# Kernel optimization log

Measured on AMD Instinct MI355X. Metric: run time of the kernel, lower is better.

The kernel has to match this reference:

```python
import jax, jax.numpy as jnp
import numpy as np
import math

H, G, DQK, DV = 16, 4, 64, 128  # n_head, n_kv_group, qk head dim, v head dim


def _rope(t):
    # t: [B, n, T, d] -- standard rotate-half RoPE, base 10000
    B, n, T, d = t.shape
    inv = 1.0 / (10000.0 ** (jnp.arange(0, d, 2, dtype=jnp.float32) / d))  # [d/2]
    ang = jnp.arange(T, dtype=jnp.float32)[:, None] * inv[None, :]          # [T, d/2]
    cos = jnp.concatenate([jnp.cos(ang), jnp.cos(ang)], axis=-1)            # [T, d]
    sin = jnp.concatenate([jnp.sin(ang), jnp.sin(ang)], axis=-1)
    t1, t2 = jnp.split(t, 2, axis=-1)
    rot = jnp.concatenate([-t2, t1], axis=-1)
    return t * cos + rot * sin


def setup_inputs() -> dict:
    key = jax.random.key(0)
    ks = jax.random.split(key, 6)
    B, T, C = 2, 2048, 1024
    x = jax.random.normal(ks[0], (B, T, C), jnp.float32)
    Wq = jax.random.normal(ks[1], (C, H * DQK), jnp.float32) * 0.02
    Wk = jax.random.normal(ks[2], (C, G * DQK), jnp.float32) * 0.02
    Wv = jax.random.normal(ks[3], (C, G * DV), jnp.float32) * 0.02
    Wproj = jax.random.normal(ks[4], (DV, C), jnp.float32) * 0.02
    lobo = jnp.full((H,), 1.0, jnp.float32)  # flash_lobo_log_const per head
    g0 = math.log2(T * T - T)                # qk_norm_factor init from block_size
    qk_norm_factor = jnp.array([g0], dtype=jnp.float32)
    return {"x": x, "iter_num": 0, "Wq": Wq, "Wk": Wk, "Wv": Wv,
            "Wproj": Wproj, "lobo": lobo, "qk_norm_factor": qk_norm_factor}


def reference(x, iter_num, Wq, Wk, Wv, Wproj, lobo, qk_norm_factor):
    B, T, C = x.shape
    # projections (bias=False)
    q = (x @ Wq).reshape(B, T, H, DQK).transpose(0, 2, 1, 3)   # [B,H,T,dqk]
    k = (x @ Wk).reshape(B, T, G, DQK).transpose(0, 2, 1, 3)   # [B,G,T,dqk]
    v = (x @ Wv).reshape(B, T, G, DV).transpose(0, 2, 1, 3)    # [B,G,T,dv]
    # rotary embeddings on q and k
    q = _rope(q)
    k = _rope(k)
    # qk-norm
    q = q / (jnp.linalg.norm(q, axis=-1, keepdims=True) + 1e-6)
    k = k / (jnp.linalg.norm(k, axis=-1, keepdims=True) + 1e-6)
    # learned logit scale: q *= g*sqrt(d), SDPA divides by sqrt(d) -> net scale g
    q = q * (qk_norm_factor[0] * jnp.sqrt(jnp.float32(DQK)))
    # GQA broadcast (repeat_interleave over kv groups)
    rep = H // G
    k = jnp.repeat(k, rep, axis=1)   # [B,H,T,dqk]
    v = jnp.repeat(v, rep, axis=1)   # [B,H,T,dv]
    logits = jnp.einsum('bhqd,bhkd->bhqk', q, k) / jnp.sqrt(jnp.float32(DQK))
    causal = jnp.tril(jnp.ones((T, T), dtype=bool))
    logits = jnp.where(causal[None, None], logits, -jnp.inf)
    # flash-lobo: zero-valued sink key, always visible, logit = per-head bias
    sink = jnp.broadcast_to(lobo[None, :, None, None], (B, H, T, 1))
    att = jax.nn.softmax(jnp.concatenate([sink, logits], axis=-1), axis=-1)
    y = jnp.einsum('bhqk,bhkd->bhqd', att[..., 1:], v)  # sink value is zero
    y = y.sum(axis=1)                                    # head-SUM merge [B,T,dv]
    return y @ Wproj                                     # [B,T,C]
```

## Files before the change

### kernel.cpp

```cpp
#include <hip/hip_runtime.h>
#include <hip/hip_bf16.h>
#include <math.h>

#define B_ 2
#define T_ 2048
#define C_ 1024
#define H_ 16
#define G_ 4
#define DQK_ 64
#define DV_ 128
#define NQKV 1792
#define KS2 2048

typedef __attribute__((ext_vector_type(8))) short short8;
typedef __attribute__((ext_vector_type(4))) float f32x4;
typedef unsigned short ushort_t;

__device__ inline ushort_t f2bf(float f) {
  union { float f; unsigned int u; } v; v.f = f;
  unsigned int r = (v.u + 0x7FFFu + ((v.u >> 16) & 1u)) >> 16;
  return (ushort_t)r;
}
__device__ inline float bf2f(ushort_t h) {
  union { unsigned int u; float f; } v; v.u = ((unsigned int)h) << 16;
  return v.f;
}

#define GLD_LDS16(g, l)                                              \
  __builtin_amdgcn_global_load_lds(                                  \
      (const __attribute__((address_space(1))) void*)(g),            \
      (__attribute__((address_space(3))) void*)(l), 16, 0, 0)

__global__ __launch_bounds__(256) void cast_x(
    const float* __restrict__ x, ushort_t* __restrict__ xb) {
  int idx = blockIdx.x * 256 + threadIdx.x;
  int m = idx >> 7;
  int c8 = idx & 127;
  const float* src = &x[(size_t)m * 1024 + c8 * 8];
  float4 v0 = *(const float4*)&src[0];
  float4 v1 = *(const float4*)&src[4];
  float f[8] = {v0.x, v0.y, v0.z, v0.w, v1.x, v1.y, v1.z, v1.w};
  short8 hv, lv;
#pragma unroll
  for (int c = 0; c < 8; c++) {
    ushort_t h = f2bf(f[c]);
    hv[c] = (short)h;
    lv[c] = (short)f2bf(f[c] - bf2f(h));
  }
  int key = (m >> 1) & 3;
  int phys = (c8 & ~3) * 8 + ((c8 & 3) ^ key) * 8;
  ushort_t* row = xb + (size_t)m * KS2;
  *(short8*)&row[phys] = hv;
  *(short8*)&row[1024 + phys] = lv;
}

__global__ __launch_bounds__(256) void cast_w(
    const float* __restrict__ Wq, const float* __restrict__ Wk,
    const float* __restrict__ Wv, ushort_t* __restrict__ wt) {
  __shared__ float tile[64][65];
  const int n0 = blockIdx.x * 64;
  const int k0 = blockIdx.y * 64;
  const int tid = threadIdx.x;

  const float* Wp; int ldw, noff;
  if (n0 < 1024)      { Wp = Wq; ldw = 1024; noff = n0; }
  else if (n0 < 1280) { Wp = Wk; ldw = 256;  noff = n0 - 1024; }
  else                { Wp = Wv; ldw = 512;  noff = n0 - 1280; }

#pragma unroll
  for (int it = 0; it < 4; it++) {
    int fi = it * 256 + tid;
    int kk = fi >> 4;
    int nc = (fi & 15) * 4;
    float4 v = *(const float4*)&Wp[(size_t)(k0 + kk) * ldw + noff + nc];
    tile[nc + 0][kk] = v.x; tile[nc + 1][kk] = v.y;
    tile[nc + 2][kk] = v.z; tile[nc + 3][kk] = v.w;
  }
  __syncthreads();
  int nn = tid >> 2, seg = tid & 3;
  int n = n0 + nn;
  int key = (n >> 1) & 3;
  ushort_t* row = wt + (size_t)n * KS2;
#pragma unroll
  for (int j = 0; j < 2; j++) {
    short8 hv;
#pragma unroll
    for (int u = 0; u < 8; u++)
      hv[u] = (short)f2bf(tile[nn][seg * 16 + j * 8 + u]);
    int c8 = (k0 >> 3) + seg * 2 + j;
    int phys = (c8 & ~3) * 8 + ((c8 & 3) ^ key) * 8;
    *(short8*)&row[phys] = hv;
  }
}

__global__ __launch_bounds__(256) void cast_wp(
    const float* __restrict__ Wp, ushort_t* __restrict__ wpf) {
  int idx = blockIdx.x * 256 + threadIdx.x;
  int n = idx & 1023;
  int kc = idx >> 10;
  short8 v;
#pragma unroll
  for (int j = 0; j < 8; j++)
    v[j] = (short)f2bf(Wp[(size_t)(kc * 8 + j) * 1024 + n]);
  size_t off = (((size_t)(n >> 7) * 4 + (kc >> 2)) * 8 + ((n >> 4) & 7)) * 512 +
               ((kc & 3) * 16 + (n & 15)) * 8;
  *(short8*)&wpf[off] = v;
}

__global__ __launch_bounds__(256) void gemm_qkv_mfma(
    const ushort_t* __restrict__ xb, const ushort_t* __restrict__ wt,
    float* __restrict__ qkv) {
  __shared__ ushort_t At[128 * 32];
  __shared__ ushort_t Bt[128 * 32];
  const int tid = threadIdx.x;
  const int wave = tid >> 6, lane = tid & 63;
  const int quad = lane >> 4, l16 = lane & 15;
  const int m0 = blockIdx.y * 128, n0 = blockIdx.x * 128;
  const int wm = (wave & 1) * 64, wn = (wave >> 1) * 64;
  const int physq = (quad ^ ((l16 >> 1) & 3)) * 8;
  const int ntiles = (n0 >= 1280) ? 32 : 64;

  f32x4 acc[4][4];
#pragma unroll
  for (int i = 0; i < 4; i++)
#pragma unroll
    for (int j = 0; j < 4; j++) acc[i][j] = (f32x4){0.f, 0.f, 0.f, 0.f};

  const int rA = wave * 32 + (lane >> 2);
  const int cA = (lane & 3) * 8;
  const ushort_t* gA = xb + (size_t)(m0 + rA) * KS2 + cA;
  const ushort_t* gB = wt + (size_t)(n0 + rA) * KS2 + cA;
  ushort_t* lA0 = At + (size_t)(wave * 32) * 32;
  ushort_t* lA1 = At + (size_t)(wave * 32 + 16) * 32;
  ushort_t* lB0 = Bt + (size_t)(wave * 32) * 32;
  ushort_t* lB1 = Bt + (size_t)(wave * 32 + 16) * 32;

  for (int kt = 0; kt < ntiles; kt++) {
    const int ca = kt * 32;
    const int cb = (kt < 32 ? kt : kt - 32) * 32;
    __syncthreads();
    GLD_LDS16(gA + ca, lA0);
    GLD_LDS16(gA + ca + 16 * KS2, lA1);
    GLD_LDS16(gB + cb, lB0);
    GLD_LDS16(gB + cb + 16 * KS2, lB1);
    __syncthreads();

    short8 af[4], bf[4];
#pragma unroll
    for (int i = 0; i < 4; i++)
      af[i] = *(const short8*)&At[(wm + 16 * i + l16) * 32 + physq];
#pragma unroll
    for (int j = 0; j < 4; j++)
      bf[j] = *(const short8*)&Bt[(wn + 16 * j + l16) * 32 + physq];
#pragma unroll
    for (int i = 0; i < 4; i++)
#pragma unroll
      for (int j = 0; j < 4; j++)
        acc[i][j] = __builtin_amdgcn_mfma_f32_16x16x32_bf16(
            af[i], bf[j], acc[i][j], 0, 0, 0);
  }

#pragma unroll
  for (int i = 0; i < 4; i++) {
    int m = m0 + wm + 16 * i + quad * 4;
#pragma unroll
    for (int j = 0; j < 4; j++) {
      int n = n0 + wn + 16 * j + l16;
#pragma unroll
      for (int r = 0; r < 4; r++)
        qkv[(size_t)(m + r) * NQKV + n] = acc[i][j][r];
    }
  }
}

__global__ __launch_bounds__(256) void rope_norm(
    const float* __restrict__ qkv,
    ushort_t* __restrict__ qf, ushort_t* __restrict__ kf) {
  const int NQ = B_ * T_ * H_;
  int vec = blockIdx.x * 4 + (threadIdx.x >> 6);
  int d = threadIdx.x & 63;

  size_t src; int t, b, isq; ushort_t* dstbase;
  if (vec < NQ) {
    int h = vec % H_; int bt = vec / H_;
    t = bt % T_; b = bt / T_;
    src = (size_t)bt * NQKV + h * 64 + d;
    dstbase = qf + (size_t)(b * 16 + h) * 131072;
    isq = 1;
  } else {
    int vk = vec - NQ;
    int g = vk % G_; int bt = vk / G_;
    t = bt % T_; b = bt / T_;
    src = (size_t)bt * NQKV + 1024 + g * 64 + d;
    dstbase = kf + (size_t)(b * 4 + g) * 131072;
    isq = 0;
  }
  float val = qkv[src];
  int i = d & 31;
  float inv = exp2f(-(float)i * 0.4152410118074239f);
  float ang = (float)t * inv;
  float sn, cs;
  __sincosf(ang, &sn, &cs);
  float partner = __shfl(val, d ^ 32, 64);
  float r = (d < 32) ? (val * cs - partner * sn) : (val * cs + partner * sn);
  float ss = r * r;
#pragma unroll
  for (int off = 32; off; off >>= 1) ss += __shfl_xor(ss, off, 64);
  r *= 1.0f / (sqrtf(ss) + 1e-6f);

  int kt = t >> 6, tt = t & 63;
  int l16v = tt & 15;
  int ks = d >> 5, quad = (d >> 3) & 3, j = d & 7;
  size_t off2;
  if (isq) {
    int wavei = tt >> 4;
    off2 = ((size_t)(kt * 8 + wavei * 2 + ks) * 4 + quad) * 128 + l16v * 8 + j;
  } else {
    int nt = tt >> 4;
    off2 = ((size_t)(kt * 8 + ks * 4 + nt) * 4 + quad) * 128 + l16v * 8 + j;
  }
  dstbase[off2] = f2bf(r);
}

__global__ __launch_bounds__(256) void vscatter(
    const float* __restrict__ qkv, ushort_t* __restrict__ vf) {
  int idx = blockIdx.x * 256 + threadIdx.x;
  int dv = idx & 127;
  int t = (idx >> 7) & 2047;
  int g = (idx >> 18) & 3;
  int b = idx >> 20;
  size_t src = (size_t)(b * T_ + t) * NQKV + 1280 + g * 128 + dv;
  float v = qkv[src];
  int kt = t >> 6, ks = (t >> 5) & 1, quad = (t >> 3) & 3, j = t & 7;
  int nv = dv >> 4, l16v = dv & 15;
  size_t off = ((size_t)(kt * 16 + ks * 8 + nv) * 4 + quad) * 128 + l16v * 8 + j;
  vf[(size_t)(b * 4 + g) * 262144 + off] = f2bf(v);
}

__global__ __launch_bounds__(256, 3) void attn(
    const ushort_t* __restrict__ qf, const ushort_t* __restrict__ kf,
    const ushort_t* __restrict__ vf, const float* __restrict__ lobo,
    const float* __restrict__ qknf, float* __restrict__ y) {
  const int f = blockIdx.x;
  const int bh = f & 31;
  const int slot = f >> 5;
  const int tq = 31 - slot;
  const int b = bh >> 4;
  const int h = bh & 15;
  const int g = h >> 2;

  __shared__ ushort_t KV[12288];
  __shared__ ushort_t Ps[4 * 1088];

  const int tid = threadIdx.x;
  const int wave = tid >> 6, lane = tid & 63;
  const int quad = lane >> 4, l16 = lane & 15;
  ushort_t* PsW = &Ps[wave * 1088];

  short8 bones;
  {
    short bv = (l16 == 0) ? (short)0x3F80 : (short)0;
#pragma unroll
    for (int j = 0; j < 8; j++) bones[j] = bv;
  }

  const ushort_t* qbase = qf + (size_t)(b * 16 + h) * 131072 + lane * 8;
  short8 aq0 = *(const short8*)&qbase[(size_t)(tq * 8 + wave * 2 + 0) * 512];
  short8 aq1 = *(const short8*)&qbase[(size_t)(tq * 8 + wave * 2 + 1) * 512];

  f32x4 o[9];
#pragma unroll
  for (int nv = 0; nv < 9; nv++) o[nv] = (f32x4){0.f, 0.f, 0.f, 0.f};

  const float gsc = qknf[0];
  const float sinkp = __expf(lobo[h] - gsc);

  const int row = tq * 64 + wave * 16 + quad * 4;

  const ushort_t* kgl = kf + (size_t)(b * 4 + g) * 131072 + lane * 8;
  const ushort_t* vgl = vf + (size_t)(b * 4 + g) * 262144 + lane * 8;

  for (int kt = 0; kt <= tq; kt++) {
    __syncthreads();
    {
      const ushort_t* gk = kgl + (size_t)kt * 4096;
      const ushort_t* gv = vgl + (size_t)kt * 8192;
      GLD_LDS16(gk + (wave * 2 + 0) * 512, &KV[(wave * 2 + 0) * 512]);
      GLD_LDS16(gk + (wave * 2 + 1) * 512, &KV[(wave * 2 + 1) * 512]);
#pragma unroll
      for (int j = 0; j < 4; j++)
        GLD_LDS16(gv + (wave * 4 + j) * 512, &KV[4096 + (wave * 4 + j) * 512]);
    }
    __syncthreads();

    f32x4 s[4];
#pragma unroll
    for (int nt = 0; nt < 4; nt++) s[nt] = (f32x4){0.f, 0.f, 0.f, 0.f};
    {
      short8 kb[4];
#pragma unroll
      for (int u = 0; u < 4; u++)
        kb[u] = *(const short8*)&KV[u * 512 + lane * 8];
      __builtin_amdgcn_s_setprio(1);
#pragma unroll
      for (int nt = 0; nt < 4; nt++)
        s[nt] = __builtin_amdgcn_mfma_f32_16x16x32_bf16(aq0, kb[nt], s[nt], 0, 0, 0);
      __builtin_amdgcn_s_setprio(0);
#pragma unroll
      for (int u = 0; u < 4; u++)
        kb[u] = *(const short8*)&KV[(4 + u) * 512 + lane * 8];
      __builtin_amdgcn_s_setprio(1);
#pragma unroll
      for (int nt = 0; nt < 4; nt++)
        s[nt] = __builtin_amdgcn_mfma_f32_16x16x32_bf16(aq1, kb[nt], s[nt], 0, 0, 0);
      __builtin_amdgcn_s_setprio(0);
    }

    if (kt == tq) {
#pragma unroll
      for (int nt = 0; nt < 4; nt++) {
        int key = kt * 64 + l16 + nt * 16;
#pragma unroll
        for (int r = 0; r < 4; r++) {
          float pv = (key <= row + r) ? __expf((s[nt][r] - 1.0f) * gsc) : 0.f;
          PsW[(quad * 4 + r) * 68 + nt * 16 + l16] = f2bf(pv);
        }
      }
    } else {
#pragma unroll
      for (int nt = 0; nt < 4; nt++)
#pragma unroll
        for (int r = 0; r < 4; r++)
          PsW[(quad * 4 + r) * 68 + nt * 16 + l16] =
              f2bf(__expf((s[nt][r] - 1.0f) * gsc));
    }

    short8 ap0 = *(const short8*)&PsW[l16 * 68 + quad * 8];
    short8 ap1 = *(const short8*)&PsW[l16 * 68 + 32 + quad * 8];
    {
      short8 vb[8];
#pragma unroll
      for (int u = 0; u < 8; u++)
        vb[u] = *(const short8*)&KV[4096 + u * 512 + lane * 8];
      __builtin_amdgcn_s_setprio(1);
#pragma unroll
      for (int nv = 0; nv < 8; nv++)
        o[nv] = __builtin_amdgcn_mfma_f32_16x16x32_bf16(ap0, vb[nv], o[nv], 0, 0, 0);
      o[8] = __builtin_amdgcn_mfma_f32_16x16x32_bf16(ap0, bones, o[8], 0, 0, 0);
      o[8] = __builtin_amdgcn_mfma_f32_16x16x32_bf16(ap1, bones, o[8], 0, 0, 0);
      __builtin_amdgcn_s_setprio(0);
#pragma unroll
      for (int u = 0; u < 8; u++)
        vb[u] = *(const short8*)&KV[4096 + (8 + u) * 512 + lane * 8];
      __builtin_amdgcn_s_setprio(1);
#pragma unroll
      for (int nv = 0; nv < 8; nv++)
        o[nv] = __builtin_amdgcn_mfma_f32_16x16x32_bf16(ap1, vb[nv], o[nv], 0, 0, 0);
      __builtin_amdgcn_s_setprio(0);
    }
  }

#pragma unroll
  for (int r = 0; r < 4; r++) {
    float lm = __shfl(o[8][r], lane & 48, 64);
    float invl = 1.0f / (lm + sinkp);
    size_t gRow = (size_t)b * T_ + row + r;
#pragma unroll
    for (int nv = 0; nv < 8; nv++)
      atomicAdd(&y[gRow * 128 + nv * 16 + l16], o[nv][r] * invl);
  }
}

__global__ __launch_bounds__(256) void out_proj(
    const float* __restrict__ y, const ushort_t* __restrict__ wpf,
    float* __restrict__ out) {
  __shared__ ushort_t yl[128 * 136];
  const int tid = threadIdx.x;
  const int wave = tid >> 6, lane = tid & 63;
  const int quad = lane >> 4, l16 = lane & 15;
  const int n0 = blockIdx.x * 128, m0 = blockIdx.y * 128;
  const int wm = (wave & 1) * 64, wn = (wave >> 1) * 64;

#pragma unroll
  for (int it = 0; it < 8; it++) {
    int p = it * 256 + tid;
    int row = p >> 4, c8 = p & 15;
    const float* src = &y[(size_t)(m0 + row) * 128 + c8 * 8];
    float4 v0 = *(const float4*)&src[0];
    float4 v1 = *(const float4*)&src[4];
    float fv[8] = {v0.x, v0.y, v0.z, v0.w, v1.x, v1.y, v1.z, v1.w};
    short8 hv;
#pragma unroll
    for (int c = 0; c < 8; c++) hv[c] = (short)f2bf(fv[c]);
    *(short8*)&yl[row * 136 + c8 * 8] = hv;
  }
  __syncthreads();

  f32x4 acc[4][4];
#pragma unroll
  for (int i = 0; i < 4; i++)
#pragma unroll
    for (int j = 0; j < 4; j++) acc[i][j] = (f32x4){0.f, 0.f, 0.f, 0.f};

#pragma unroll
  for (int ks = 0; ks < 4; ks++) {
    short8 af[4], bfr[4];
#pragma unroll
    for (int i = 0; i < 4; i++)
      af[i] = *(const short8*)&yl[(wm + 16 * i + l16) * 136 + (ks * 4 + quad) * 8];
    const ushort_t* wb = wpf + (((size_t)(n0 >> 7) * 4 + ks) * 8) * 512;
#pragma unroll
    for (int j = 0; j < 4; j++)
      bfr[j] = *(const short8*)&wb[((size_t)((wn >> 4) + j)) * 512 + lane * 8];
#pragma unroll
    for (int i = 0; i < 4; i++)
#pragma unroll
      for (int j = 0; j < 4; j++)
        acc[i][j] = __builtin_amdgcn_mfma_f32_16x16x32_bf16(
            af[i], bfr[j], acc[i][j], 0, 0, 0);
  }

#pragma unroll
  for (int i = 0; i < 4; i++) {
    int m = m0 + wm + 16 * i + quad * 4;
#pragma unroll
    for (int j = 0; j < 4; j++) {
      int n = n0 + wn + 16 * j + l16;
#pragma unroll
      for (int r = 0; r < 4; r++)
        out[(size_t)(m + r) * 1024 + n] = acc[i][j][r];
    }
  }
}

extern "C" void kernel_launch(void* const* d_in, const int* in_sizes, int n_in,
                              void* d_out, int out_size, void* d_ws, size_t ws_size,
                              hipStream_t stream) {
  const float* x     = (const float*)d_in[0];
  const float* Wq    = (const float*)d_in[2];
  const float* Wk    = (const float*)d_in[3];
  const float* Wv    = (const float*)d_in[4];
  const float* Wproj = (const float*)d_in[5];
  const float* lobo  = (const float*)d_in[6];
  const float* qknf  = (const float*)d_in[7];
  float* out = (float*)d_out;

  float* qkv = (float*)d_ws;
  ushort_t* xb = (ushort_t*)(qkv + (size_t)B_ * T_ * NQKV);
  ushort_t* wt = xb + (size_t)B_ * T_ * KS2;
  ushort_t* wpf = wt + (size_t)NQKV * KS2;
  ushort_t* qf = xb;
  ushort_t* kf = qf + (size_t)B_ * H_ * T_ * 64;
  ushort_t* vf = kf + (size_t)B_ * G_ * T_ * 64;
  float* y = (float*)(vf + (size_t)B_ * G_ * T_ * 128);

  cast_x<<<(B_ * T_ * 128) / 256, 256, 0, stream>>>(x, xb);
  dim3 gw(NQKV / 64, C_ / 64);
  cast_w<<<gw, 256, 0, stream>>>(Wq, Wk, Wv, wt);
  cast_wp<<<64, 256, 0, stream>>>(Wproj, wpf);

  dim3 gg(NQKV / 128, (B_ * T_) / 128);
  gemm_qkv_mfma<<<gg, 256, 0, stream>>>(xb, wt, qkv);

  int nvec = B_ * T_ * H_ + B_ * T_ * G_;
  rope_norm<<<nvec / 4, 256, 0, stream>>>(qkv, qf, kf);

  vscatter<<<(B_ * G_ * T_ * DV_) / 256, 256, 0, stream>>>(qkv, vf);

  (void)hipMemsetAsync(y, 0, (size_t)B_ * T_ * 128 * sizeof(float), stream);

  attn<<<B_ * H_ * 32, 256, 0, stream>>>(qf, kf, vf, lobo, qknf, y);

  dim3 go(8, 32);
  out_proj<<<go, 256, 0, stream>>>(y, wpf, out);
}
```

Before: 240.9 us.

## Double-buffer K/V tiles in LDS to overlap loads with attention compute

The attention kernel now keeps two LDS buffers for K/V tiles. It prefetches the next tile with direct global-to-LDS loads while the current tile runs through the MFMA work, so there is one barrier per iteration instead of two. The goal is to hide global load latency behind compute. In exchange LDS use roughly doubles and the occupancy hint drops from 3 to 2 blocks per CU, which may reduce latency hiding across waves.

Measured after the change: 246.4 us. +2.3%, slower.

```diff
diff --git a/kernel.cpp b/kernel.cpp
--- a/kernel.cpp
+++ b/kernel.cpp
@@ -237,7 +237,7 @@
   vf[(size_t)(b * 4 + g) * 262144 + off] = f2bf(v);
 }
 
-__global__ __launch_bounds__(256, 3) void attn(
+__global__ __launch_bounds__(256, 2) void attn(
     const ushort_t* __restrict__ qf, const ushort_t* __restrict__ kf,
     const ushort_t* __restrict__ vf, const float* __restrict__ lobo,
     const float* __restrict__ qknf, float* __restrict__ y) {
@@ -249,7 +249,7 @@
   const int h = bh & 15;
   const int g = h >> 2;
 
-  __shared__ ushort_t KV[12288];
+  __shared__ ushort_t KV[2][12288];
   __shared__ ushort_t Ps[4 * 1088];
 
   const int tid = threadIdx.x;
@@ -280,18 +280,29 @@
   const ushort_t* kgl = kf + (size_t)(b * 4 + g) * 131072 + lane * 8;
   const ushort_t* vgl = vf + (size_t)(b * 4 + g) * 262144 + lane * 8;
 
+  {
+    ushort_t* KVn = &KV[0][0];
+    GLD_LDS16(kgl + (wave * 2 + 0) * 512, &KVn[(wave * 2 + 0) * 512]);
+    GLD_LDS16(kgl + (wave * 2 + 1) * 512, &KVn[(wave * 2 + 1) * 512]);
+#pragma unroll
+    for (int j = 0; j < 4; j++)
+      GLD_LDS16(vgl + (wave * 4 + j) * 512, &KVn[4096 + (wave * 4 + j) * 512]);
+  }
+  __syncthreads();
+
   for (int kt = 0; kt <= tq; kt++) {
-    __syncthreads();
-    {
-      const ushort_t* gk = kgl + (size_t)kt * 4096;
-      const ushort_t* gv = vgl + (size_t)kt * 8192;
-      GLD_LDS16(gk + (wave * 2 + 0) * 512, &KV[(wave * 2 + 0) * 512]);
-      GLD_LDS16(gk + (wave * 2 + 1) * 512, &KV[(wave * 2 + 1) * 512]);
+    ushort_t* KVc = &KV[kt & 1][0];
+
+    if (kt < tq) {
+      ushort_t* KVn = &KV[(kt + 1) & 1][0];
+      const ushort_t* gk = kgl + (size_t)(kt + 1) * 4096;
+      const ushort_t* gv = vgl + (size_t)(kt + 1) * 8192;
+      GLD_LDS16(gk + (wave * 2 + 0) * 512, &KVn[(wave * 2 + 0) * 512]);
+      GLD_LDS16(gk + (wave * 2 + 1) * 512, &KVn[(wave * 2 + 1) * 512]);
 #pragma unroll
       for (int j = 0; j < 4; j++)
-        GLD_LDS16(gv + (wave * 4 + j) * 512, &KV[4096 + (wave * 4 + j) * 512]);
-    }
-    __syncthreads();
+        GLD_LDS16(gv + (wave * 4 + j) * 512, &KVn[4096 + (wave * 4 + j) * 512]);
+    }
 
     f32x4 s[4];
 #pragma unroll
@@ -300,7 +311,7 @@
       short8 kb[4];
 #pragma unroll
       for (int u = 0; u < 4; u++)
-        kb[u] = *(const short8*)&KV[u * 512 + lane * 8];
+        kb[u] = *(const short8*)&KVc[u * 512 + lane * 8];
       __builtin_amdgcn_s_setprio(1);
 #pragma unroll
       for (int nt = 0; nt < 4; nt++)
@@ -308,7 +319,7 @@
       __builtin_amdgcn_s_setprio(0);
 #pragma unroll
       for (int u = 0; u < 4; u++)
-        kb[u] = *(const short8*)&KV[(4 + u) * 512 + lane * 8];
+        kb[u] = *(const short8*)&KVc[(4 + u) * 512 + lane * 8];
       __builtin_amdgcn_s_setprio(1);
 #pragma unroll
       for (int nt = 0; nt < 4; nt++)
@@ -341,7 +352,7 @@
       short8 vb[8];
 #pragma unroll
       for (int u = 0; u < 8; u++)
-        vb[u] = *(const short8*)&KV[4096 + u * 512 + lane * 8];
+        vb[u] = *(const short8*)&KVc[4096 + u * 512 + lane * 8];
       __builtin_amdgcn_s_setprio(1);
 #pragma unroll
       for (int nv = 0; nv < 8; nv++)
@@ -351,13 +362,15 @@
       __builtin_amdgcn_s_setprio(0);
 #pragma unroll
       for (int u = 0; u < 8; u++)
-        vb[u] = *(const short8*)&KV[4096 + (8 + u) * 512 + lane * 8];
+        vb[u] = *(const short8*)&KVc[4096 + (8 + u) * 512 + lane * 8];
       __builtin_amdgcn_s_setprio(1);
 #pragma unroll
       for (int nv = 0; nv < 8; nv++)
         o[nv] = __builtin_amdgcn_mfma_f32_16x16x32_bf16(ap1, vb[nv], o[nv], 0, 0, 0);
       __builtin_amdgcn_s_setprio(0);
     }
+
+    __syncthreads();
   }
 
 #pragma unroll
```
